# Optimization experiments

Measured on AMD Instinct MI355X. Metric: run time of the kernel, lower is better.

## Reference

```python
import jax, jax.numpy as jnp
import numpy as np

EMBED_DIM = 512
NUM_HEADS = 8
HEAD_DIM = EMBED_DIM // NUM_HEADS
GRID_SHAPE = (48, 48)
WINDOW = (16, 16)
BATCH = 2
SEQ = GRID_SHAPE[0] * GRID_SHAPE[1]
NEG = float(np.finfo(np.float16).min)  # matches torch.finfo(torch.float16).min fill


def build_window_mask():
    # replicates: indices = np.indices(grid).flatten(1).T; dist = |i-j|*2; all(dist < window)
    idx = np.indices(GRID_SHAPE).reshape(len(GRID_SHAPE), -1).T  # [N, 2]
    dist = np.abs(idx[:, None, :] - idx[None, :, :]) * 2          # [N, N, 2]
    mask = np.all(dist < np.array(WINDOW)[None, None, :], axis=-1)  # [N, N] bool
    return jnp.asarray(mask)


def setup_inputs() -> dict:
    key = jax.random.key(0)
    ks = jax.random.split(key, 11)
    s = 1.0 / np.sqrt(EMBED_DIM)
    inp = {
        "x_q": jax.random.normal(ks[0], (BATCH, SEQ, EMBED_DIM), jnp.float32),
        "x_k": jax.random.normal(ks[1], (BATCH, SEQ, EMBED_DIM), jnp.float32),
        "x_v": jax.random.normal(ks[2], (BATCH, SEQ, EMBED_DIM), jnp.float32),
        "Wq": jax.random.normal(ks[3], (EMBED_DIM, EMBED_DIM), jnp.float32) * s,
        "bq": jnp.zeros((EMBED_DIM,), jnp.float32),
        "Wk": jax.random.normal(ks[4], (EMBED_DIM, EMBED_DIM), jnp.float32) * s,
        "bk": jnp.zeros((EMBED_DIM,), jnp.float32),
        "Wv": jax.random.normal(ks[5], (EMBED_DIM, EMBED_DIM), jnp.float32) * s,
        "bv": jnp.zeros((EMBED_DIM,), jnp.float32),
        "Wo": jax.random.normal(ks[6], (EMBED_DIM, EMBED_DIM), jnp.float32) * s,
        "bo": jnp.zeros((EMBED_DIM,), jnp.float32),
        "attn_mask": build_window_mask(),
    }
    return inp


def reference(x_q, x_k, x_v, Wq, bq, Wk, bk, Wv, bv, Wo, bo, attn_mask):
    B, S, E = x_q.shape
    H, D = NUM_HEADS, HEAD_DIM

    def proj(x, W, b):
        y = x @ W.T + b                         # [B,S,E]
        return y.reshape(B, S, H, D).transpose(0, 2, 1, 3)  # [B,H,S,D]

    q = proj(x_q, Wq, bq)
    k = proj(x_k, Wk, bk)
    v = proj(x_v, Wv, bv)

    scores = jnp.einsum("bhqd,bhkd->bhqk", q, k) / np.sqrt(D)
    # Windowed branch: per-row gather over allowed keys + softmax == dense
    # softmax with disallowed keys masked to a huge negative value.
    scores = jnp.where(attn_mask[None, None, :, :], scores, NEG)
    probs = jax.nn.softmax(scores, axis=-1)     # dropout=0.0 -> identity
    context = jnp.einsum("bhqk,bhkd->bhqd", probs, v)
    context = context.transpose(0, 2, 1, 3).reshape(B, S, E)
    out = context @ Wo.T + bo
    return out
```

## Files before the change

### kernel.cpp

```cpp
#include <hip/hip_runtime.h>

typedef __attribute__((ext_vector_type(8))) short short8;
typedef __attribute__((ext_vector_type(4))) float f32x4;
typedef __attribute__((ext_vector_type(2))) unsigned int u32x2;
typedef __attribute__((ext_vector_type(4))) unsigned int u32x4;

#define DEV __device__ __forceinline__

#define XQ_E 0L
#define XK_E 2359296L
#define XV_E 4718592L
#define WQ_E 7077888L
#define WK_E 7340032L
#define WV_E 7602176L
#define QH_E 7864320L
#define KH_E 10223616L
#define VT_E 12582912L
#define CTX_E 14942208L

#define LOG2E 1.4426950408889634f

#define BARRIER() __builtin_amdgcn_s_barrier()
#define SCHED0() __builtin_amdgcn_sched_barrier(0)

DEV unsigned short f2bf(float f) {
  unsigned int x = __float_as_uint(f);
  x = (x + 0x7fffu + ((x >> 16) & 1u)) >> 16;
  return (unsigned short)x;
}

DEV unsigned int pk2(float a, float b) {
  unsigned int r;
  asm("v_cvt_pk_bf16_f32 %0, %1, %2" : "=v"(r) : "v"(a), "v"(b));
  return r;
}

DEV void gl2lds16(const unsigned short* g, unsigned short* l) {
  __builtin_amdgcn_global_load_lds(
      (const __attribute__((address_space(1))) unsigned int*)g,
      (__attribute__((address_space(3))) unsigned int*)l, 16, 0, 0);
}

DEV f32x4 mfma16(short8 a, short8 b, f32x4 c) {
  return __builtin_amdgcn_mfma_f32_16x16x32_bf16(a, b, c, 0, 0, 0);
}

__global__ __launch_bounds__(256) void cvt_kernel(
    const float* __restrict__ xq, const float* __restrict__ xk,
    const float* __restrict__ xv, const float* __restrict__ wq,
    const float* __restrict__ wk, const float* __restrict__ wv,
    unsigned short* __restrict__ ws) {
  int t = blockIdx.x * 256 + threadIdx.x;
  const float* src;
  long rel, dstE;
  float sc = 1.0f;
  if (t < 1769472) {
    if (t < 589824)       { src = xq; rel = t;            dstE = XQ_E; }
    else if (t < 1179648) { src = xk; rel = t - 589824;   dstE = XK_E; }
    else                  { src = xv; rel = t - 1179648;  dstE = XV_E; }
  } else {
    int u = t - 1769472;
    if (u < 65536)        { src = wq; rel = u;            dstE = WQ_E; sc = 0.125f * LOG2E; }
    else if (u < 131072)  { src = wk; rel = u - 65536;    dstE = WK_E; }
    else                  { src = wv; rel = u - 131072;   dstE = WV_E; }
  }
  f32x4 v = *(const f32x4*)(src + rel * 4);
  v *= sc;
  u32x2 o;
  o.x = pk2(v.x, v.y);
  o.y = pk2(v.z, v.w);
  *(u32x2*)(ws + dstE + rel * 4) = o;
}

__global__ __launch_bounds__(512, 6) void proj_qkv_kernel(
    unsigned short* __restrict__ ws, const float* __restrict__ bq,
    const float* __restrict__ bk, const float* __restrict__ bv) {
  __shared__ unsigned short ldsA[3 * 4096];
  __shared__ unsigned short ldsB[3 * 4096];
  int f = blockIdx.x;
  int wid = (f & 7) * 54 + (f >> 3);
  const int z = wid / 144;
  const int rem = wid % 144;
  const int m0 = (rem >> 2) * 128, n0 = (rem & 3) * 128;
  const unsigned short *A, *W;
  const float* bias;
  unsigned short* dst;
  float bscale;
  int mode;
  if (z == 0)      { A = ws + XQ_E; W = ws + WQ_E; bias = bq; bscale = 0.125f * LOG2E; dst = ws + QH_E; mode = 0; }
  else if (z == 1) { A = ws + XK_E; W = ws + WK_E; bias = bk; bscale = 1.0f;           dst = ws + KH_E; mode = 0; }
  else             { A = ws + XV_E; W = ws + WV_E; bias = bv; bscale = 1.0f;           dst = ws + VT_E; mode = 1; }
  const int tid = threadIdx.x;
  const int lane = tid & 63, wvv = tid >> 6;
  const int g = lane >> 4, qi = lane & 15;
  const int wr = wvv >> 2, wc = wvv & 3;
  const int srow = tid >> 2, sc8 = tid & 3;
  f32x4 acc[4][2];
#pragma unroll
  for (int mi = 0; mi < 4; ++mi)
#pragma unroll
    for (int ni = 0; ni < 2; ++ni) {
      f32x4 z4 = {0.f, 0.f, 0.f, 0.f};
      acc[mi][ni] = z4;
    }
#define STG(bi, kt) do {                                                      \
    const long k0_ = (long)(kt) * 32 + sc8 * 8;                               \
    gl2lds16(A + (long)(m0 + srow) * 512 + k0_, ldsA + (bi) * 4096 + tid * 8);\
    gl2lds16(W + (long)(n0 + srow) * 512 + k0_, ldsB + (bi) * 4096 + tid * 8);\
  } while (0)
  STG(0, 0);
  STG(1, 1);
#pragma unroll
  for (int t = 0; t < 16; ++t) {
    if (t < 15) { asm volatile("s_waitcnt vmcnt(2)" ::: "memory"); }
    else        { asm volatile("s_waitcnt vmcnt(0)" ::: "memory"); }
    BARRIER();
    SCHED0();
    if (t + 2 < 16) STG((t + 2) % 3, t + 2);
    const unsigned short* La = ldsA + (t % 3) * 4096;
    const unsigned short* Lb = ldsB + (t % 3) * 4096;
    __builtin_amdgcn_s_setprio(1);
    short8 af[4], bfr[2];
#pragma unroll
    for (int mi = 0; mi < 4; ++mi)
      af[mi] = *(const short8*)(La + (64 * wr + 16 * mi + qi) * 32 + g * 8);
#pragma unroll
    for (int ni = 0; ni < 2; ++ni)
      bfr[ni] = *(const short8*)(Lb + (32 * wc + 16 * ni + qi) * 32 + g * 8);
#pragma unroll
    for (int mi = 0; mi < 4; ++mi)
#pragma unroll
      for (int ni = 0; ni < 2; ++ni)
        acc[mi][ni] = mfma16(af[mi], bfr[ni], acc[mi][ni]);
    __builtin_amdgcn_s_setprio(0);
    SCHED0();
  }
#undef STG
#pragma unroll
  for (int ni = 0; ni < 2; ++ni) {
    int n = n0 + 32 * wc + 16 * ni + qi;
    float bb = bias[n] * bscale;
    int h = n >> 6, d = n & 63;
#pragma unroll
    for (int mi = 0; mi < 4; ++mi) {
      int m = m0 + 64 * wr + 16 * mi + 4 * g;
      int b = (m >= 2304) ? 1 : 0;
      int s = m - b * 2304;
      if (mode == 0) {
#pragma unroll
        for (int r = 0; r < 4; ++r) {
          float v = acc[mi][ni][r] + bb;
          dst[((long)((b * 8 + h) * 2304 + s + r)) * 64 + d] = f2bf(v);
        }
      } else {
        u32x2 o;
        o.x = pk2(acc[mi][ni][0] + bb, acc[mi][ni][1] + bb);
        o.y = pk2(acc[mi][ni][2] + bb, acc[mi][ni][3] + bb);
        *(u32x2*)(dst + ((long)((b * 8 + h) * 64 + d)) * 2304 + s) = o;
      }
    }
  }
}

DEV void gemm_o(const unsigned short* __restrict__ A, const float* __restrict__ W,
                int m0, int n0, unsigned short* ldsA, unsigned short* ldsB,
                f32x4 acc[2][2]) {
  const int tid = threadIdx.x;
  const int lane = tid & 63, wvv = tid >> 6;
  const int g = lane >> 4, qi = lane & 15;
  const int wr = wvv >> 1, wc = wvv & 1;
  const int c8 = tid & 7, rbase = tid >> 3;
  const int j8 = (c8 ^ (rbase & 7)) * 8;
  u32x4 rab[2][2];
  f32x4 rw[2][2][2];
#pragma unroll
  for (int mi = 0; mi < 2; ++mi)
#pragma unroll
    for (int ni = 0; ni < 2; ++ni) {
      f32x4 z = {0.f, 0.f, 0.f, 0.f};
      acc[mi][ni] = z;
    }
#define OLA(kt) do {                                                          \
    const int k0_ = (kt) * 64;                                                \
    _Pragma("unroll")                                                         \
    for (int it = 0; it < 2; ++it)                                            \
      rab[(kt) & 1][it] =                                                     \
          *(const u32x4*)(A + (long)(m0 + it * 32 + rbase) * 512 + k0_ + j8); \
  } while (0)
#define OLB(kt) do {                                                          \
    const int k0_ = (kt) * 64;                                                \
    _Pragma("unroll")                                                         \
    for (int it = 0; it < 2; ++it) {                                          \
      const float* p = W + (long)(n0 + it * 32 + rbase) * 512 + k0_ + j8;     \
      rw[(kt) & 1][it][0] = *(const f32x4*)p;                                 \
      rw[(kt) & 1][it][1] = *(const f32x4*)(p + 4);                           \
    }                                                                         \
  } while (0)
#define OW(kt) do {                                                           \
    const int b3_ = (kt) % 3, s_ = (kt) & 1;                                  \
    _Pragma("unroll")                                                         \
    for (int it = 0; it < 2; ++it)                                            \
      *(u32x4*)(ldsA + b3_ * 4096 + (it * 256 + tid) * 8) = rab[s_][it];      \
    _Pragma("unroll")                                                         \
    for (int it = 0; it < 2; ++it) {                                          \
      u32x4 v_;                                                               \
      v_.x = pk2(rw[s_][it][0].x, rw[s_][it][0].y);                           \
      v_.y = pk2(rw[s_][it][0].z, rw[s_][it][0].w);                           \
      v_.z = pk2(rw[s_][it][1].x, rw[s_][it][1].y);                           \
      v_.w = pk2(rw[s_][it][1].z, rw[s_][it][1].w);                           \
      *(u32x4*)(ldsB + b3_ * 4096 + (it * 256 + tid) * 8) = v_;               \
    }                                                                         \
  } while (0)
  OLA(0); OLB(0);
  OLA(1); OLB(1);
  OW(0);
  OLA(2); OLB(2);
  OW(1);
  OLA(3); OLB(3);
  asm volatile("s_waitcnt lgkmcnt(0)" ::: "memory");
  BARRIER();
  SCHED0();
#pragma unroll
  for (int kt = 0; kt < 8; ++kt) {
    const unsigned short* La = ldsA + (kt % 3) * 4096;
    const unsigned short* Lb = ldsB + (kt % 3) * 4096;
    __builtin_amdgcn_s_setprio(1);
#pragma unroll
    for (int kk = 0; kk < 2; ++kk) {
      short8 af[2], bfr[2];
#pragma unroll
      for (int mi = 0; mi < 2; ++mi) {
        int row = 32 * wr + 16 * mi + qi;
        int c16 = (4 * kk + g) ^ (qi & 7);
        af[mi] = *(const short8*)(La + row * 64 + c16 * 8);
      }
#pragma unroll
      for (int ni = 0; ni < 2; ++ni) {
        int row = 32 * wc + 16 * ni + qi;
        int c16 = (4 * kk + g) ^ (qi & 7);
        bfr[ni] = *(const short8*)(Lb + row * 64 + c16 * 8);
      }
#pragma unroll
      for (int mi = 0; mi < 2; ++mi)
#pragma unroll
        for (int ni = 0; ni < 2; ++ni)
          acc[mi][ni] = mfma16(af[mi], bfr[ni], acc[mi][ni]);
    }
    __builtin_amdgcn_s_setprio(0);
    SCHED0();
    if (kt < 6) OW(kt + 2);
    if (kt < 4) { OLA(kt + 4); OLB(kt + 4); }
    if (kt < 7) {
      asm volatile("s_waitcnt lgkmcnt(0)" ::: "memory");
      BARRIER();
      SCHED0();
    }
  }
#undef OLA
#undef OLB
#undef OW
}

__global__ __launch_bounds__(256, 3) void proj_out_kernel(
    const unsigned short* __restrict__ ws, const float* __restrict__ wop,
    const float* __restrict__ bo, float* __restrict__ out) {
  __shared__ unsigned short ldsA[3 * 4096];
  __shared__ unsigned short ldsB[3 * 4096];
  int f = blockIdx.x;
  int wid = (f & 7) * 72 + (f >> 3);
  const int m0 = (wid >> 3) * 64, n0 = (wid & 7) * 64;
  f32x4 acc[2][2];
  gemm_o(ws + CTX_E, wop, m0, n0, ldsA, ldsB, acc);
  const int lane = threadIdx.x & 63, wvv = threadIdx.x >> 6;
  const int g = lane >> 4, qi = lane & 15;
  const int wr = wvv >> 1, wc = wvv & 1;
#pragma unroll
  for (int ni = 0; ni < 2; ++ni) {
    int n = n0 + 32 * wc + 16 * ni + qi;
    float bb = bo[n];
#pragma unroll
    for (int mi = 0; mi < 2; ++mi) {
#pragma unroll
      for (int r = 0; r < 4; ++r) {
        int m = m0 + 32 * wr + 16 * mi + 4 * g + r;
        out[(long)m * 512 + n] = acc[mi][ni][r] + bb;
      }
    }
  }
}

__global__ __launch_bounds__(192) void attn_kernel(unsigned short* __restrict__ ws) {
  __shared__ unsigned short ldsKV[3 * 7168];
  __shared__ unsigned short ldsP[3][16][72];
  __shared__ unsigned short ldsDum[512];
  const int tid = threadIdx.x;
  const int lane = tid & 63, wv = tid >> 6;
  const int g = lane >> 4, qi = lane & 15;
  int f = blockIdx.x;
  int wid = (f & 7) * 96 + (f >> 3);
  const int bh = wid / 48, r = wid - 48 * bh;
  const int ci = wv * 16 + qi;
  const unsigned short* Kh = ws + KH_E + (long)bh * 2304 * 64;
  const unsigned short* Vt = ws + VT_E + (long)bh * 64 * 2304;
  const int q = r * 48 + ci;
  const unsigned short* qp = ws + QH_E + ((long)bh * 2304 + q) * 64;
  f32x4 qraw0 = *(const f32x4*)(qp + 8 * g);
  f32x4 qraw1 = *(const f32x4*)(qp + 32 + 8 * g);
  asm volatile("" : "+v"(qraw0), "+v"(qraw1));
  short8 qf0 = __builtin_bit_cast(short8, qraw0);
  short8 qf1 = __builtin_bit_cast(short8, qraw1);
  float msk[12];
#pragma unroll
  for (int mb = 0; mb < 3; ++mb)
#pragma unroll
    for (int rr = 0; rr < 4; ++rr) {
      int cj = 16 * mb + 4 * g + rr;
      msk[mb * 4 + rr] = ((unsigned)(ci - cj + 7) <= 14u) ? 0.f : -1e30f;
    }
  {
    u32x2 z2; z2.x = 0u; z2.y = 0u;
    *(u32x2*)(&ldsP[wv][qi][48 + 4 * g]) = z2;
  }
  f32x4 cacc[4];
#pragma unroll
  for (int mb = 0; mb < 4; ++mb) { f32x4 z = {0.f, 0.f, 0.f, 0.f}; cacc[mb] = z; }
  float lrun = 0.f;

#define ASTAGE(bi, rj) do {                                                   \
    unsigned short* Lb_ = ldsKV + (bi) * 7168;                                \
    const unsigned short* Ks_ = Kh + (long)(rj) * 3072;                       \
    _Pragma("unroll")                                                         \
    for (int it = 0; it < 5; ++it) {                                          \
      int u = it * 192 + tid;                                                 \
      if (u < 384) {                                                          \
        int kr = u >> 3, c = u & 7, cs = c ^ (kr & 7);                        \
        gl2lds16(Ks_ + kr * 64 + cs * 8, Lb_ + u * 8);                        \
      } else if (u < 896) {                                                   \
        int v2 = u - 384;                                                     \
        int d = v2 >> 3, c = v2 & 7, cs = c ^ (d & 7);                        \
        long jb = (long)(rj) * 48 + cs * 8;                                   \
        if (jb > 2296) jb = 2296;                                             \
        gl2lds16(Vt + (long)d * 2304 + jb, Lb_ + u * 8);                      \
      } else {                                                                \
        gl2lds16(Kh + (u - 896) * 8, ldsDum + (u - 896) * 8);                 \
      }                                                                       \
    }                                                                         \
  } while (0)

  const int rlo = (r > 7) ? r - 7 : 0;
  const int rhi = (r < 40) ? r + 7 : 47;
  const int nch = rhi - rlo + 1;
  ASTAGE(0, rlo);
  ASTAGE(1, rlo + 1);
  for (int t = 0; t < nch; ++t) {
    if (t + 1 < nch) { asm volatile("s_waitcnt vmcnt(5)" ::: "memory"); }
    else             { asm volatile("s_waitcnt vmcnt(0)" ::: "memory"); }
    BARRIER();
    SCHED0();
    if (t + 2 < nch) ASTAGE((t + 2) % 3, rlo + t + 2);
    const unsigned short* Kt = ldsKV + (t % 3) * 7168;
    const unsigned short* Vm = Kt + 3072;
    f32x4 sacc[3];
#pragma unroll
    for (int mb = 0; mb < 3; ++mb) { f32x4 z = {0.f, 0.f, 0.f, 0.f}; sacc[mb] = z; }
    __builtin_amdgcn_s_setprio(1);
#pragma unroll
    for (int kk = 0; kk < 2; ++kk) {
      short8 qf_ = kk ? qf1 : qf0;
#pragma unroll
      for (int mb = 0; mb < 3; ++mb) {
        int row = 16 * mb + qi;
        int c16 = (4 * kk + g) ^ (qi & 7);
        short8 ka = *(const short8*)(Kt + row * 64 + c16 * 8);
        sacc[mb] = mfma16(ka, qf_, sacc[mb]);
      }
    }
    __builtin_amdgcn_s_setprio(0);
    unsigned int pw[6];
#pragma unroll
    for (int mb = 0; mb < 3; ++mb) {
      float p0 = __builtin_amdgcn_exp2f(sacc[mb][0] + msk[mb * 4 + 0]);
      float p1 = __builtin_amdgcn_exp2f(sacc[mb][1] + msk[mb * 4 + 1]);
      float p2 = __builtin_amdgcn_exp2f(sacc[mb][2] + msk[mb * 4 + 2]);
      float p3 = __builtin_amdgcn_exp2f(sacc[mb][3] + msk[mb * 4 + 3]);
      lrun += (p0 + p1) + (p2 + p3);
      pw[2 * mb] = pk2(p0, p1);
      pw[2 * mb + 1] = pk2(p2, p3);
    }
#pragma unroll
    for (int mb = 0; mb < 3; ++mb) {
      u32x2 pv2; pv2.x = pw[2 * mb]; pv2.y = pw[2 * mb + 1];
      *(u32x2*)(&ldsP[wv][qi][16 * mb + 4 * g]) = pv2;
    }
    __builtin_amdgcn_s_setprio(1);
#pragma unroll
    for (int kk = 0; kk < 2; ++kk) {
      short8 pb = *(const short8*)(&ldsP[wv][qi][32 * kk + 8 * g]);
#pragma unroll
      for (int mb = 0; mb < 4; ++mb) {
        int row = 16 * mb + qi;
        int c16 = (4 * kk + g) ^ (qi & 7);
        short8 va = *(const short8*)(Vm + row * 64 + c16 * 8);
        cacc[mb] = mfma16(va, pb, cacc[mb]);
      }
    }
    __builtin_amdgcn_s_setprio(0);
  }
#undef ASTAGE
  lrun += __shfl_xor(lrun, 16);
  lrun += __shfl_xor(lrun, 32);
  const float inv = 1.0f / lrun;
  unsigned short* ctx = ws + CTX_E;
  const int b2w = bh >> 3, h2 = bh & 7;
#pragma unroll
  for (int mb = 0; mb < 4; ++mb) {
    u32x2 o;
    o.x = pk2(cacc[mb][0] * inv, cacc[mb][1] * inv);
    o.y = pk2(cacc[mb][2] * inv, cacc[mb][3] * inv);
    long off = ((long)(b2w * 2304 + q)) * 512 + h2 * 64 + 16 * mb + 4 * g;
    *(u32x2*)(ctx + off) = o;
  }
}

extern "C" void kernel_launch(void* const* d_in, const int* in_sizes, int n_in,
                              void* d_out, int out_size, void* d_ws, size_t ws_size,
                              hipStream_t stream) {
  const float* xq = (const float*)d_in[0];
  const float* xk = (const float*)d_in[1];
  const float* xv = (const float*)d_in[2];
  const float* wq = (const float*)d_in[3];
  const float* bq = (const float*)d_in[4];
  const float* wk = (const float*)d_in[5];
  const float* bk = (const float*)d_in[6];
  const float* wv = (const float*)d_in[7];
  const float* bv = (const float*)d_in[8];
  const float* wo = (const float*)d_in[9];
  const float* bo = (const float*)d_in[10];
  unsigned short* ws = (unsigned short*)d_ws;
  float* out = (float*)d_out;

  cvt_kernel<<<dim3(7680), dim3(256), 0, stream>>>(xq, xk, xv, wq, wk, wv, ws);
  proj_qkv_kernel<<<dim3(432), dim3(512), 0, stream>>>(ws, bq, bk, bv);
  attn_kernel<<<dim3(768), dim3(192), 0, stream>>>(ws);
  proj_out_kernel<<<dim3(576), dim3(256), 0, stream>>>(ws, wo, bo, out);
}
```

Baseline: 60.56 us.

## Restructure QKV projection GEMM to 4 waves, BK=64, XOR-swizzled LDS, double buffer

The QKV projection kernel moves from 8 waves with 4x2 MFMA tiles per wave to 4 waves with 4x4 tiles per wave. The K step doubles to 64, so each tile takes 8 iterations instead of 16. LDS staging now uses an XOR swizzle on 16-byte chunks to avoid bank conflicts and drops from triple to double buffering. The aim is more register-level reuse per wave, fewer barriers and fewer LDS conflicts. The cost is fewer waves per CU to hide latency and a full vmcnt(0) wait every iteration, which gives less load/compute overlap.

```diff
diff --git a/kernel.cpp b/kernel.cpp
--- a/kernel.cpp
+++ b/kernel.cpp
@@ -72,11 +72,11 @@
   *(u32x2*)(ws + dstE + rel * 4) = o;
 }
 
-__global__ __launch_bounds__(512, 6) void proj_qkv_kernel(
+__global__ __launch_bounds__(256, 2) void proj_qkv_kernel(
     unsigned short* __restrict__ ws, const float* __restrict__ bq,
     const float* __restrict__ bk, const float* __restrict__ bv) {
-  __shared__ unsigned short ldsA[3 * 4096];
-  __shared__ unsigned short ldsB[3 * 4096];
+  __shared__ unsigned short ldsA[2 * 8192];
+  __shared__ unsigned short ldsB[2 * 8192];
   int f = blockIdx.x;
   int wid = (f & 7) * 54 + (f >> 3);
   const int z = wid / 144;
@@ -93,52 +93,60 @@
   const int tid = threadIdx.x;
   const int lane = tid & 63, wvv = tid >> 6;
   const int g = lane >> 4, qi = lane & 15;
-  const int wr = wvv >> 2, wc = wvv & 3;
-  const int srow = tid >> 2, sc8 = tid & 3;
-  f32x4 acc[4][2];
+  const int wr = wvv >> 1, wc = wvv & 1;
+  f32x4 acc[4][4];
 #pragma unroll
   for (int mi = 0; mi < 4; ++mi)
 #pragma unroll
-    for (int ni = 0; ni < 2; ++ni) {
+    for (int ni = 0; ni < 4; ++ni) {
       f32x4 z4 = {0.f, 0.f, 0.f, 0.f};
       acc[mi][ni] = z4;
     }
 #define STG(bi, kt) do {                                                      \
-    const long k0_ = (long)(kt) * 32 + sc8 * 8;                               \
-    gl2lds16(A + (long)(m0 + srow) * 512 + k0_, ldsA + (bi) * 4096 + tid * 8);\
-    gl2lds16(W + (long)(n0 + srow) * 512 + k0_, ldsB + (bi) * 4096 + tid * 8);\
+    const long k0_ = (long)(kt) * 64;                                         \
+    _Pragma("unroll")                                                         \
+    for (int it = 0; it < 4; ++it) {                                          \
+      int idx = it * 256 + tid;                       \
+      int row = idx >> 3, c = idx & 7, cs = c ^ (row & 7);                    \
+      gl2lds16(A + (long)(m0 + row) * 512 + k0_ + cs * 8,                     \
+               ldsA + (bi) * 8192 + idx * 8);                                 \
+      gl2lds16(W + (long)(n0 + row) * 512 + k0_ + cs * 8,                     \
+               ldsB + (bi) * 8192 + idx * 8);                                 \
+    }                                                                         \
   } while (0)
   STG(0, 0);
-  STG(1, 1);
-#pragma unroll
-  for (int t = 0; t < 16; ++t) {
-    if (t < 15) { asm volatile("s_waitcnt vmcnt(2)" ::: "memory"); }
-    else        { asm volatile("s_waitcnt vmcnt(0)" ::: "memory"); }
+#pragma unroll
+  for (int kt = 0; kt < 8; ++kt) {
+    asm volatile("s_waitcnt vmcnt(0)" ::: "memory");
     BARRIER();
     SCHED0();
-    if (t + 2 < 16) STG((t + 2) % 3, t + 2);
-    const unsigned short* La = ldsA + (t % 3) * 4096;
-    const unsigned short* Lb = ldsB + (t % 3) * 4096;
+    if (kt + 1 < 8) STG((kt + 1) & 1, kt + 1);
+    const unsigned short* La = ldsA + (kt & 1) * 8192;
+    const unsigned short* Lb = ldsB + (kt & 1) * 8192;
     __builtin_amdgcn_s_setprio(1);
-    short8 af[4], bfr[2];
-#pragma unroll
-    for (int mi = 0; mi < 4; ++mi)
-      af[mi] = *(const short8*)(La + (64 * wr + 16 * mi + qi) * 32 + g * 8);
-#pragma unroll
-    for (int ni = 0; ni < 2; ++ni)
-      bfr[ni] = *(const short8*)(Lb + (32 * wc + 16 * ni + qi) * 32 + g * 8);
-#pragma unroll
-    for (int mi = 0; mi < 4; ++mi)
-#pragma unroll
-      for (int ni = 0; ni < 2; ++ni)
-        acc[mi][ni] = mfma16(af[mi], bfr[ni], acc[mi][ni]);
+#pragma unroll
+    for (int kk = 0; kk < 2; ++kk) {
+      short8 af[4], bfr[4];
+      int c16 = (4 * kk + g) ^ (qi & 7);
+#pragma unroll
+      for (int mi = 0; mi < 4; ++mi)
+        af[mi] = *(const short8*)(La + (64 * wr + 16 * mi + qi) * 64 + c16 * 8);
+#pragma unroll
+      for (int ni = 0; ni < 4; ++ni)
+        bfr[ni] = *(const short8*)(Lb + (64 * wc + 16 * ni + qi) * 64 + c16 * 8);
+#pragma unroll
+      for (int mi = 0; mi < 4; ++mi)
+#pragma unroll
+        for (int ni = 0; ni < 4; ++ni)
+          acc[mi][ni] = mfma16(af[mi], bfr[ni], acc[mi][ni]);
+    }
     __builtin_amdgcn_s_setprio(0);
     SCHED0();
   }
 #undef STG
 #pragma unroll
-  for (int ni = 0; ni < 2; ++ni) {
-    int n = n0 + 32 * wc + 16 * ni + qi;
+  for (int ni = 0; ni < 4; ++ni) {
+    int n = n0 + 64 * wc + 16 * ni + qi;
     float bb = bias[n] * bscale;
     int h = n >> 6, d = n & 63;
 #pragma unroll
@@ -440,7 +448,7 @@
   float* out = (float*)d_out;
 
   cvt_kernel<<<dim3(7680), dim3(256), 0, stream>>>(xq, xk, xv, wq, wk, wv, ws);
-  proj_qkv_kernel<<<dim3(432), dim3(512), 0, stream>>>(ws, bq, bk, bv);
+  proj_qkv_kernel<<<dim3(432), dim3(256), 0, stream>>>(ws, bq, bk, bv);
   attn_kernel<<<dim3(768), dim3(192), 0, stream>>>(ws);
   proj_out_kernel<<<dim3(576), dim3(256), 0, stream>>>(ws, wo, bo, out);
 }
```

Result: faster. 58.58 us (-3.3%).
